# Kernel optimization log

Hardware: AMD Instinct MI355X
Metric: run time of the kernel (lower is better)

Reference implementation:

```python
import jax, jax.numpy as jnp
import numpy as np

ALPHA = 0.2  # LeakyReLU negative slope

def setup_inputs() -> dict:
    key = jax.random.key(0)
    k1, k2, k3 = jax.random.split(key, 3)
    B, N, D_in, D_out = 4, 512, 512, 256
    H = jax.random.normal(k1, (B, N, D_in), dtype=jnp.float32)
    # xavier-style scaled params
    W = jax.random.normal(k2, (D_out, D_in), dtype=jnp.float32) * (2.0 / (D_in + D_out)) ** 0.5
    a = jax.random.normal(k3, (D_out, 1), dtype=jnp.float32) * (2.0 / (D_out + 1)) ** 0.5
    return {"H": H, "W": W, "a": a}

def reference(H, W, a):
    # Wh: [B, N, D_out]
    Wh = jnp.einsum('bnd,od->bno', H, W)
    # additive pairwise scores: e[b,i,j] = leakyrelu(Wh[b,i]+Wh[b,j]) . a
    e = jnp.einsum('bijo,o->bij',
                   jax.nn.leaky_relu(Wh[:, :, None, :] + Wh[:, None, :, :], ALPHA),
                   a[:, 0])
    attention = jax.nn.softmax(e, axis=-1)          # [B, N, N]
    H_att = jnp.einsum('bij,bjo->bio', attention, Wh)  # [B, N, D_out]
    return H_att
```

## Files before the change

### kernel.cpp

```cpp
#include <hip/hip_runtime.h>

constexpr int Bq   = 4;
constexpr int Nq   = 512;
constexpr int DIN  = 512;
constexpr int DOUT = 256;

__device__ __forceinline__ void fma4(float4& acc, const float s, const float4 v) {
    acc.x = __builtin_fmaf(s, v.x, acc.x);
    acc.y = __builtin_fmaf(s, v.y, acc.y);
    acc.z = __builtin_fmaf(s, v.z, acc.z);
    acc.w = __builtin_fmaf(s, v.w, acc.w);
}

__global__ __launch_bounds__(256) void k0_wt(const float* __restrict__ W,
                                             float* __restrict__ WT) {
    __shared__ float tile[32][33];
    const int k0 = blockIdx.x * 32;
    const int o0 = blockIdx.y * 32;
    const int tx = threadIdx.x;
    const int ty = threadIdx.y;
#pragma unroll
    for (int j = 0; j < 4; ++j)
        tile[ty + 8 * j][tx] = W[(o0 + ty + 8 * j) * DIN + k0 + tx];
    __syncthreads();
#pragma unroll
    for (int j = 0; j < 4; ++j)
        WT[(k0 + ty + 8 * j) * DOUT + o0 + tx] = tile[tx][ty + 8 * j];
}

__global__ __launch_bounds__(512, 4) void k1_wh(const float* __restrict__ H,
                                                const float* __restrict__ WT,
                                                const float* __restrict__ a,
                                                float* __restrict__ Wh,
                                                float* __restrict__ WhT,
                                                float* __restrict__ r) {
    const int t   = threadIdx.x;
    const int blk = blockIdx.x;
    const int b   = blk & 3;
    const int n0  = (blk >> 2) << 2;
    const int p   = __builtin_amdgcn_readfirstlane(t >> 6);
    const int oq  = t & 63;

    __shared__ float  sH[4 * 512];
    __shared__ float4 sPart[8][4][64];

    {
        const float4* src = (const float4*)(H + ((size_t)(b * Nq) + n0) * DIN);
        ((float4*)sH)[t] = src[t];
    }
    __syncthreads();

    const float4* __restrict__ wt4 = (const float4*)WT + oq;

    float4 acc[4];
#pragma unroll
    for (int rr = 0; rr < 4; ++rr) acc[rr] = make_float4(0.f, 0.f, 0.f, 0.f);

    const int k0 = p * 64;
    float4 bufA[4], bufB[4];
#pragma unroll
    for (int s = 0; s < 4; ++s) bufA[s] = wt4[(k0 + s) * 64];

    for (int it = 0; it < 8; ++it) {
        const int kA = k0 + it * 8, kB = kA + 4;
#pragma unroll
        for (int s = 0; s < 4; ++s) bufB[s] = wt4[(kB + s) * 64];
#pragma unroll
        for (int rr = 0; rr < 4; ++rr) {
            const float4 h4 = *(const float4*)&sH[rr * 512 + kA];
            fma4(acc[rr], h4.x, bufA[0]); fma4(acc[rr], h4.y, bufA[1]);
            fma4(acc[rr], h4.z, bufA[2]); fma4(acc[rr], h4.w, bufA[3]);
        }
        if (it < 7) {
#pragma unroll
            for (int s = 0; s < 4; ++s) bufA[s] = wt4[(kA + 8 + s) * 64];
        }
#pragma unroll
        for (int rr = 0; rr < 4; ++rr) {
            const float4 h4 = *(const float4*)&sH[rr * 512 + kB];
            fma4(acc[rr], h4.x, bufB[0]); fma4(acc[rr], h4.y, bufB[1]);
            fma4(acc[rr], h4.z, bufB[2]); fma4(acc[rr], h4.w, bufB[3]);
        }
    }

#pragma unroll
    for (int rr = 0; rr < 4; ++rr) sPart[p][rr][oq] = acc[rr];
    __syncthreads();

    if (p < 4) {
        const int g = p;
        float4 fin = make_float4(0.f, 0.f, 0.f, 0.f);
#pragma unroll
        for (int pp = 0; pp < 8; ++pp) {
            const float4 v = sPart[pp][g][oq];
            fin.x += v.x; fin.y += v.y; fin.z += v.z; fin.w += v.w;
        }

        ((float4*)(Wh + ((size_t)(b * Nq) + n0 + g) * DOUT))[oq] = fin;

        float* wT = WhT + (size_t)b * DOUT * Nq;
        wT[(4 * oq + 0) * Nq + n0 + g] = fin.x;
        wT[(4 * oq + 1) * Nq + n0 + g] = fin.y;
        wT[(4 * oq + 2) * Nq + n0 + g] = fin.z;
        wT[(4 * oq + 3) * Nq + n0 + g] = fin.w;

        const float4 a4 = ((const float4*)a)[oq];
        float rp = a4.x * fin.x + a4.y * fin.y + a4.z * fin.z + a4.w * fin.w;
#pragma unroll
        for (int off = 32; off > 0; off >>= 1) rp += __shfl_xor(rp, off);
        if ((t & 63) == 0) r[(size_t)b * Nq + n0 + g] = rp;
    }
}

__global__ __launch_bounds__(1024, 4) void k2_attn(const float* __restrict__ Wh,
                                                   const float* __restrict__ WhT,
                                                   const float* __restrict__ a,
                                                   const float* __restrict__ r,
                                                   float* __restrict__ P) {
    const int t   = threadIdx.x;
    const int blk = blockIdx.x;
    const int b   = blk & 3;
    const int i0  = (blk >> 2) << 3;
    const int q   = __builtin_amdgcn_readfirstlane(t >> 8);
    const int jp  = t & 255;
    const int obase = q * 64;

    const float2* __restrict__ wj2 =
        (const float2*)(WhT + (size_t)b * DOUT * Nq + (size_t)obase * Nq) + jp;
    const float* __restrict__ gwi = Wh + ((size_t)b * Nq + i0) * DOUT;
    const float* __restrict__ gr  = r + (size_t)b * Nq;

    float ab0[8] = {0.f, 0.f, 0.f, 0.f, 0.f, 0.f, 0.f, 0.f};
    float ab1[8] = {0.f, 0.f, 0.f, 0.f, 0.f, 0.f, 0.f, 0.f};
    float2 bufA[8], bufB[8];

#pragma unroll
    for (int s = 0; s < 8; ++s) bufA[s] = wj2[s * 256];

    for (int cc = 0; cc < 4; ++cc) {
        const int oA = cc * 16, oB = oA + 8;
#pragma unroll
        for (int s = 0; s < 8; ++s) bufB[s] = wj2[(oB + s) * 256];
#pragma unroll
        for (int gg = 0; gg < 2; ++gg) {
            const int o4 = obase + oA + gg * 4;
            const float4 a4 = *(const float4*)(a + o4);
#pragma unroll
            for (int rr = 0; rr < 8; ++rr) {
                const float4 wi4 = *(const float4*)(gwi + rr * DOUT + o4);
#pragma unroll
                for (int s2 = 0; s2 < 4; ++s2) {
                    const float aq = ((const float*)&a4)[s2];
                    const float wi = ((const float*)&wi4)[s2];
                    const float2 wv = bufA[gg * 4 + s2];
                    ab0[rr] = __builtin_fmaf(aq, __builtin_fabsf(wi + wv.x), ab0[rr]);
                    ab1[rr] = __builtin_fmaf(aq, __builtin_fabsf(wi + wv.y), ab1[rr]);
                }
            }
        }
        if (cc < 3) {
#pragma unroll
            for (int s = 0; s < 8; ++s) bufA[s] = wj2[(oA + 16 + s) * 256];
        }
#pragma unroll
        for (int gg = 0; gg < 2; ++gg) {
            const int o4 = obase + oB + gg * 4;
            const float4 a4 = *(const float4*)(a + o4);
#pragma unroll
            for (int rr = 0; rr < 8; ++rr) {
                const float4 wi4 = *(const float4*)(gwi + rr * DOUT + o4);
#pragma unroll
                for (int s2 = 0; s2 < 4; ++s2) {
                    const float aq = ((const float*)&a4)[s2];
                    const float wi = ((const float*)&wi4)[s2];
                    const float2 wv = bufB[gg * 4 + s2];
                    ab0[rr] = __builtin_fmaf(aq, __builtin_fabsf(wi + wv.x), ab0[rr]);
                    ab1[rr] = __builtin_fmaf(aq, __builtin_fabsf(wi + wv.y), ab1[rr]);
                }
            }
        }
    }

    __shared__ float sAb[3][8][512];
    __shared__ float wred[2][8][4];
    if (q > 0) {
#pragma unroll
        for (int rr = 0; rr < 8; ++rr)
            ((float2*)&sAb[q - 1][rr][0])[jp] = make_float2(ab0[rr], ab1[rr]);
    }
    __syncthreads();

    float e0[8], e1[8];
    if (q == 0) {
        const float2 rj2 = ((const float2*)gr)[jp];
#pragma unroll
        for (int rr = 0; rr < 8; ++rr) {
            const float2 x0 = ((const float2*)&sAb[0][rr][0])[jp];
            const float2 x1 = ((const float2*)&sAb[1][rr][0])[jp];
            const float2 x2 = ((const float2*)&sAb[2][rr][0])[jp];
            const float A0 = ab0[rr] + x0.x + x1.x + x2.x;
            const float A1 = ab1[rr] + x0.y + x1.y + x2.y;
            const float ri = gr[i0 + rr];
            e0[rr] = 0.6f * (ri + rj2.x) + 0.4f * A0;
            e1[rr] = 0.6f * (ri + rj2.y) + 0.4f * A1;
        }
    }

    const int lane = t & 63;
    const int w    = (t >> 6) & 3;

#pragma unroll
    for (int rr = 0; rr < 8; ++rr) {
        float v = (q == 0) ? fmaxf(e0[rr], e1[rr]) : -3e38f;
#pragma unroll
        for (int off = 32; off > 0; off >>= 1) v = fmaxf(v, __shfl_xor(v, off));
        if (lane == 0 && q == 0) wred[0][rr][w] = v;
    }
    __syncthreads();

    float p0[8], p1[8];
    if (q == 0) {
#pragma unroll
        for (int rr = 0; rr < 8; ++rr) {
            const float4 qv = *(const float4*)&wred[0][rr][0];
            const float m = fmaxf(fmaxf(qv.x, qv.y), fmaxf(qv.z, qv.w));
            p0[rr] = __expf(e0[rr] - m);
            p1[rr] = __expf(e1[rr] - m);
        }
    }
#pragma unroll
    for (int rr = 0; rr < 8; ++rr) {
        float v = (q == 0) ? (p0[rr] + p1[rr]) : 0.f;
#pragma unroll
        for (int off = 32; off > 0; off >>= 1) v += __shfl_xor(v, off);
        if (lane == 0 && q == 0) wred[1][rr][w] = v;
    }
    __syncthreads();

    if (q == 0) {
        float2* prow = (float2*)(P + ((size_t)b * Nq + i0) * Nq) + jp;
#pragma unroll
        for (int rr = 0; rr < 8; ++rr) {
            const float4 qv = *(const float4*)&wred[1][rr][0];
            const float inv = 1.0f / (qv.x + qv.y + qv.z + qv.w);
            prow[rr * 256] = make_float2(p0[rr] * inv, p1[rr] * inv);
        }
    }
}

__global__ __launch_bounds__(512, 4) void k3_av(const float* __restrict__ Wh,
                                                const float* __restrict__ P,
                                                float* __restrict__ out) {
    const int t   = threadIdx.x;
    const int blk = blockIdx.x;
    const int b   = blk & 3;
    const int i0  = (blk >> 2) << 2;
    const int p   = __builtin_amdgcn_readfirstlane(t >> 6);
    const int oq  = t & 63;

    __shared__ float  sP[4 * 512];
    __shared__ float4 sPart[8][4][64];

    {
        const float4* src = (const float4*)(P + ((size_t)(b * Nq) + i0) * Nq);
        ((float4*)sP)[t] = src[t];
    }
    __syncthreads();

    const float4* __restrict__ wh4 = (const float4*)(Wh + (size_t)b * Nq * DOUT) + oq;

    float4 acc[4];
#pragma unroll
    for (int rr = 0; rr < 4; ++rr) acc[rr] = make_float4(0.f, 0.f, 0.f, 0.f);

    const int j0 = p * 64;
    float4 bufA[4], bufB[4];
#pragma unroll
    for (int s = 0; s < 4; ++s) bufA[s] = wh4[(j0 + s) * 64];

    for (int it = 0; it < 8; ++it) {
        const int jA = j0 + it * 8, jB = jA + 4;
#pragma unroll
        for (int s = 0; s < 4; ++s) bufB[s] = wh4[(jB + s) * 64];
#pragma unroll
        for (int rr = 0; rr < 4; ++rr) {
            const float4 p4 = *(const float4*)&sP[rr * 512 + jA];
            fma4(acc[rr], p4.x, bufA[0]); fma4(acc[rr], p4.y, bufA[1]);
            fma4(acc[rr], p4.z, bufA[2]); fma4(acc[rr], p4.w, bufA[3]);
        }
        if (it < 7) {
#pragma unroll
            for (int s = 0; s < 4; ++s) bufA[s] = wh4[(jA + 8 + s) * 64];
        }
#pragma unroll
        for (int rr = 0; rr < 4; ++rr) {
            const float4 p4 = *(const float4*)&sP[rr * 512 + jB];
            fma4(acc[rr], p4.x, bufB[0]); fma4(acc[rr], p4.y, bufB[1]);
            fma4(acc[rr], p4.z, bufB[2]); fma4(acc[rr], p4.w, bufB[3]);
        }
    }

#pragma unroll
    for (int rr = 0; rr < 4; ++rr) sPart[p][rr][oq] = acc[rr];
    __syncthreads();

    if (p < 4) {
        const int g = p;
        float4 fin = make_float4(0.f, 0.f, 0.f, 0.f);
#pragma unroll
        for (int pp = 0; pp < 8; ++pp) {
            const float4 v = sPart[pp][g][oq];
            fin.x += v.x; fin.y += v.y; fin.z += v.z; fin.w += v.w;
        }
        ((float4*)(out + ((size_t)(b * Nq) + i0 + g) * DOUT))[oq] = fin;
    }
}

extern "C" void kernel_launch(void* const* d_in, const int* in_sizes, int n_in,
                              void* d_out, int out_size, void* d_ws, size_t ws_size,
                              hipStream_t stream) {
    const float* H = (const float*)d_in[0];
    const float* W = (const float*)d_in[1];
    const float* a = (const float*)d_in[2];
    float* out = (float*)d_out;

    float* Wh  = (float*)d_ws;
    float* WhT = Wh  + Bq * Nq * DOUT;
    float* P   = WhT + Bq * Nq * DOUT;
    float* WT  = P;
    float* r   = out;

    hipLaunchKernelGGL(k0_wt,   dim3(16, 8), dim3(32, 8), 0, stream, W, WT);
    hipLaunchKernelGGL(k1_wh,   dim3(512),   dim3(512),   0, stream, H, WT, a, Wh, WhT, r);
    hipLaunchKernelGGL(k2_attn, dim3(256),   dim3(1024),  0, stream, Wh, WhT, a, r, P);
    hipLaunchKernelGGL(k3_av,   dim3(512),   dim3(512),   0, stream, Wh, P, out);
}
```

Measured before the change: 121.9 us.

## Fuse attention scores, softmax and attention-value product into one kernel

```diff
diff --git a/kernel.cpp b/kernel.cpp
--- a/kernel.cpp
+++ b/kernel.cpp
@@ -5,11 +5,12 @@
 constexpr int DIN  = 512;
 constexpr int DOUT = 256;
 
-__device__ __forceinline__ void fma4(float4& acc, const float s, const float4 v) {
-    acc.x = __builtin_fmaf(s, v.x, acc.x);
-    acc.y = __builtin_fmaf(s, v.y, acc.y);
-    acc.z = __builtin_fmaf(s, v.z, acc.z);
-    acc.w = __builtin_fmaf(s, v.w, acc.w);
+typedef float v2f __attribute__((ext_vector_type(2)));
+typedef float v4f __attribute__((ext_vector_type(4)));
+
+__device__ __forceinline__ v4f fma4v(const float s, const v4f v, const v4f acc) {
+    v4f sv = s;
+    return __builtin_elementwise_fma(sv, v, acc);
 }
 
 __global__ __launch_bounds__(256) void k0_wt(const float* __restrict__ W,
@@ -41,23 +42,23 @@
     const int p   = __builtin_amdgcn_readfirstlane(t >> 6);
     const int oq  = t & 63;
 
-    __shared__ float  sH[4 * 512];
-    __shared__ float4 sPart[8][4][64];
+    __shared__ float sH[4 * 512];
+    __shared__ v4f   sPart[8][4][64];
 
     {
-        const float4* src = (const float4*)(H + ((size_t)(b * Nq) + n0) * DIN);
-        ((float4*)sH)[t] = src[t];
+        const v4f* src = (const v4f*)(H + ((size_t)(b * Nq) + n0) * DIN);
+        ((v4f*)sH)[t] = src[t];
     }
     __syncthreads();
 
-    const float4* __restrict__ wt4 = (const float4*)WT + oq;
-
-    float4 acc[4];
-#pragma unroll
-    for (int rr = 0; rr < 4; ++rr) acc[rr] = make_float4(0.f, 0.f, 0.f, 0.f);
+    const v4f* __restrict__ wt4 = (const v4f*)WT + oq;
+
+    v4f acc[4];
+#pragma unroll
+    for (int rr = 0; rr < 4; ++rr) acc[rr] = (v4f)0.f;
 
     const int k0 = p * 64;
-    float4 bufA[4], bufB[4];
+    v4f bufA[4], bufB[4];
 #pragma unroll
     for (int s = 0; s < 4; ++s) bufA[s] = wt4[(k0 + s) * 64];
 
@@ -67,9 +68,11 @@
         for (int s = 0; s < 4; ++s) bufB[s] = wt4[(kB + s) * 64];
 #pragma unroll
         for (int rr = 0; rr < 4; ++rr) {
-            const float4 h4 = *(const float4*)&sH[rr * 512 + kA];
-            fma4(acc[rr], h4.x, bufA[0]); fma4(acc[rr], h4.y, bufA[1]);
-            fma4(acc[rr], h4.z, bufA[2]); fma4(acc[rr], h4.w, bufA[3]);
+            const v4f h4 = *(const v4f*)&sH[rr * 512 + kA];
+            acc[rr] = fma4v(h4.x, bufA[0], acc[rr]);
+            acc[rr] = fma4v(h4.y, bufA[1], acc[rr]);
+            acc[rr] = fma4v(h4.z, bufA[2], acc[rr]);
+            acc[rr] = fma4v(h4.w, bufA[3], acc[rr]);
         }
         if (it < 7) {
 #pragma unroll
@@ -77,9 +80,11 @@
         }
 #pragma unroll
         for (int rr = 0; rr < 4; ++rr) {
-            const float4 h4 = *(const float4*)&sH[rr * 512 + kB];
-            fma4(acc[rr], h4.x, bufB[0]); fma4(acc[rr], h4.y, bufB[1]);
-            fma4(acc[rr], h4.z, bufB[2]); fma4(acc[rr], h4.w, bufB[3]);
+            const v4f h4 = *(const v4f*)&sH[rr * 512 + kB];
+            acc[rr] = fma4v(h4.x, bufB[0], acc[rr]);
+            acc[rr] = fma4v(h4.y, bufB[1], acc[rr]);
+            acc[rr] = fma4v(h4.z, bufB[2], acc[rr]);
+            acc[rr] = fma4v(h4.w, bufB[3], acc[rr]);
         }
     }
 
@@ -89,14 +94,11 @@
 
     if (p < 4) {
         const int g = p;
-        float4 fin = make_float4(0.f, 0.f, 0.f, 0.f);
-#pragma unroll
-        for (int pp = 0; pp < 8; ++pp) {
-            const float4 v = sPart[pp][g][oq];
-            fin.x += v.x; fin.y += v.y; fin.z += v.z; fin.w += v.w;
-        }
-
-        ((float4*)(Wh + ((size_t)(b * Nq) + n0 + g) * DOUT))[oq] = fin;
+        v4f fin = (v4f)0.f;
+#pragma unroll
+        for (int pp = 0; pp < 8; ++pp) fin += sPart[pp][g][oq];
+
+        ((v4f*)(Wh + ((size_t)(b * Nq) + n0 + g) * DOUT))[oq] = fin;
 
         float* wT = WhT + (size_t)b * DOUT * Nq;
         wT[(4 * oq + 0) * Nq + n0 + g] = fin.x;
@@ -104,7 +106,7 @@
         wT[(4 * oq + 2) * Nq + n0 + g] = fin.z;
         wT[(4 * oq + 3) * Nq + n0 + g] = fin.w;
 
-        const float4 a4 = ((const float4*)a)[oq];
+        const v4f a4 = ((const v4f*)a)[oq];
         float rp = a4.x * fin.x + a4.y * fin.y + a4.z * fin.z + a4.w * fin.w;
 #pragma unroll
         for (int off = 32; off > 0; off >>= 1) rp += __shfl_xor(rp, off);
@@ -112,207 +114,220 @@
     }
 }
 
-__global__ __launch_bounds__(1024, 4) void k2_attn(const float* __restrict__ Wh,
-                                                   const float* __restrict__ WhT,
-                                                   const float* __restrict__ a,
-                                                   const float* __restrict__ r,
-                                                   float* __restrict__ P) {
+__global__ __launch_bounds__(1024, 4) void k23(const float* __restrict__ Wh,
+                                               const float* __restrict__ WhT,
+                                               const float* __restrict__ a,
+                                               const float* __restrict__ r,
+                                               float* __restrict__ out) {
     const int t   = threadIdx.x;
     const int blk = blockIdx.x;
     const int b   = blk & 3;
     const int i0  = (blk >> 2) << 3;
-    const int q   = __builtin_amdgcn_readfirstlane(t >> 8);
-    const int jp  = t & 255;
-    const int obase = q * 64;
-
-    const float2* __restrict__ wj2 =
-        (const float2*)(WhT + (size_t)b * DOUT * Nq + (size_t)obase * Nq) + jp;
-    const float* __restrict__ gwi = Wh + ((size_t)b * Nq + i0) * DOUT;
-    const float* __restrict__ gr  = r + (size_t)b * Nq;
-
-    float ab0[8] = {0.f, 0.f, 0.f, 0.f, 0.f, 0.f, 0.f, 0.f};
-    float ab1[8] = {0.f, 0.f, 0.f, 0.f, 0.f, 0.f, 0.f, 0.f};
-    float2 bufA[8], bufB[8];
-
-#pragma unroll
-    for (int s = 0; s < 8; ++s) bufA[s] = wj2[s * 256];
-
-    for (int cc = 0; cc < 4; ++cc) {
-        const int oA = cc * 16, oB = oA + 8;
-#pragma unroll
-        for (int s = 0; s < 8; ++s) bufB[s] = wj2[(oB + s) * 256];
-#pragma unroll
-        for (int gg = 0; gg < 2; ++gg) {
-            const int o4 = obase + oA + gg * 4;
-            const float4 a4 = *(const float4*)(a + o4);
+
+    __shared__ float smem[8192];
+    __shared__ float sP[8 * 512];
+    __shared__ float wred[2][8][4];
+
+    {
+        const int q  = __builtin_amdgcn_readfirstlane(t >> 8);
+        const int jp = t & 255;
+        const int obase = q * 64;
+
+        const v2f* __restrict__ wj2 =
+            (const v2f*)(WhT + (size_t)b * DOUT * Nq + (size_t)obase * Nq) + jp;
+        const float* __restrict__ gwi = Wh + ((size_t)b * Nq + i0) * DOUT;
+        const float* __restrict__ gr  = r + (size_t)b * Nq;
+
+        v2f ab[8];
+#pragma unroll
+        for (int rr = 0; rr < 8; ++rr) ab[rr] = (v2f)0.f;
+        v2f bufA[8], bufB[8];
+
+#pragma unroll
+        for (int s = 0; s < 8; ++s) bufA[s] = wj2[s * 256];
+
+        for (int cc = 0; cc < 4; ++cc) {
+            const int oA = cc * 16, oB = oA + 8;
+#pragma unroll
+            for (int s = 0; s < 8; ++s) bufB[s] = wj2[(oB + s) * 256];
+#pragma unroll
+            for (int gg = 0; gg < 2; ++gg) {
+                const int o4 = obase + oA + gg * 4;
+                const float4 a4 = *(const float4*)(a + o4);
+#pragma unroll
+                for (int rr = 0; rr < 8; ++rr) {
+                    const float4 wi4 = *(const float4*)(gwi + rr * DOUT + o4);
+#pragma unroll
+                    for (int s2 = 0; s2 < 4; ++s2) {
+                        const float aq = ((const float*)&a4)[s2];
+                        const float wi = ((const float*)&wi4)[s2];
+                        v2f w  = bufA[gg * 4 + s2] + wi;
+                        v2f aw = __builtin_elementwise_max(w, -w);
+                        v2f av = aq;
+                        ab[rr] = __builtin_elementwise_fma(av, aw, ab[rr]);
+                    }
+                }
+            }
+            if (cc < 3) {
+#pragma unroll
+                for (int s = 0; s < 8; ++s) bufA[s] = wj2[(oA + 16 + s) * 256];
+            }
+#pragma unroll
+            for (int gg = 0; gg < 2; ++gg) {
+                const int o4 = obase + oB + gg * 4;
+                const float4 a4 = *(const float4*)(a + o4);
+#pragma unroll
+                for (int rr = 0; rr < 8; ++rr) {
+                    const float4 wi4 = *(const float4*)(gwi + rr * DOUT + o4);
+#pragma unroll
+                    for (int s2 = 0; s2 < 4; ++s2) {
+                        const float aq = ((const float*)&a4)[s2];
+                        const float wi = ((const float*)&wi4)[s2];
+                        v2f w  = bufB[gg * 4 + s2] + wi;
+                        v2f aw = __builtin_elementwise_max(w, -w);
+                        v2f av = aq;
+                        ab[rr] = __builtin_elementwise_fma(av, aw, ab[rr]);
+                    }
+                }
+            }
+        }
+
+        v2f* sAb = (v2f*)smem;
+        if (q >= 2) {
+#pragma unroll
+            for (int rr = 0; rr < 8; ++rr) sAb[((q - 2) * 8 + rr) * 256 + jp] = ab[rr];
+        }
+        __syncthreads();
+        if (q < 2) {
+#pragma unroll
+            for (int rr = 0; rr < 8; ++rr) ab[rr] += sAb[(q * 8 + rr) * 256 + jp];
+        }
+        __syncthreads();
+        if (q == 1) {
+#pragma unroll
+            for (int rr = 0; rr < 8; ++rr) sAb[(0 * 8 + rr) * 256 + jp] = ab[rr];
+        }
+        __syncthreads();
+
+        float e0[8], e1[8];
+        if (q == 0) {
+            const v2f rj2 = ((const v2f*)gr)[jp];
 #pragma unroll
             for (int rr = 0; rr < 8; ++rr) {
-                const float4 wi4 = *(const float4*)(gwi + rr * DOUT + o4);
-#pragma unroll
-                for (int s2 = 0; s2 < 4; ++s2) {
-                    const float aq = ((const float*)&a4)[s2];
-                    const float wi = ((const float*)&wi4)[s2];
-                    const float2 wv = bufA[gg * 4 + s2];
-                    ab0[rr] = __builtin_fmaf(aq, __builtin_fabsf(wi + wv.x), ab0[rr]);
-                    ab1[rr] = __builtin_fmaf(aq, __builtin_fabsf(wi + wv.y), ab1[rr]);
-                }
-            }
-        }
-        if (cc < 3) {
-#pragma unroll
-            for (int s = 0; s < 8; ++s) bufA[s] = wj2[(oA + 16 + s) * 256];
-        }
-#pragma unroll
-        for (int gg = 0; gg < 2; ++gg) {
-            const int o4 = obase + oB + gg * 4;
-            const float4 a4 = *(const float4*)(a + o4);
+                const v2f x = sAb[(0 * 8 + rr) * 256 + jp];
+                const float A0 = ab[rr].x + x.x;
+                const float A1 = ab[rr].y + x.y;
+                const float ri = gr[i0 + rr];
+                e0[rr] = 0.6f * (ri + rj2.x) + 0.4f * A0;
+                e1[rr] = 0.6f * (ri + rj2.y) + 0.4f * A1;
+            }
+        }
+
+        const int lane = t & 63;
+        const int w    = (t >> 6) & 3;
+
+#pragma unroll
+        for (int rr = 0; rr < 8; ++rr) {
+            float v = (q == 0) ? fmaxf(e0[rr], e1[rr]) : -3e38f;
+#pragma unroll
+            for (int off = 32; off > 0; off >>= 1) v = fmaxf(v, __shfl_xor(v, off));
+            if (lane == 0 && q == 0) wred[0][rr][w] = v;
+        }
+        __syncthreads();
+
+        float p0[8], p1[8];
+        if (q == 0) {
 #pragma unroll
             for (int rr = 0; rr < 8; ++rr) {
-                const float4 wi4 = *(const float4*)(gwi + rr * DOUT + o4);
-#pragma unroll
-                for (int s2 = 0; s2 < 4; ++s2) {
-                    const float aq = ((const float*)&a4)[s2];
-                    const float wi = ((const float*)&wi4)[s2];
-                    const float2 wv = bufB[gg * 4 + s2];
-                    ab0[rr] = __builtin_fmaf(aq, __builtin_fabsf(wi + wv.x), ab0[rr]);
-                    ab1[rr] = __builtin_fmaf(aq, __builtin_fabsf(wi + wv.y), ab1[rr]);
-                }
-            }
-        }
-    }
-
-    __shared__ float sAb[3][8][512];
-    __shared__ float wred[2][8][4];
-    if (q > 0) {
-#pragma unroll
-        for (int rr = 0; rr < 8; ++rr)
-            ((float2*)&sAb[q - 1][rr][0])[jp] = make_float2(ab0[rr], ab1[rr]);
-    }
-    __syncthreads();
-
-    float e0[8], e1[8];
-    if (q == 0) {
-        const float2 rj2 = ((const float2*)gr)[jp];
+                const float4 qv = *(const float4*)&wred[0][rr][0];
+                const float m = fmaxf(fmaxf(qv.x, qv.y), fmaxf(qv.z, qv.w));
+                p0[rr] = __expf(e0[rr] - m);
+                p1[rr] = __expf(e1[rr] - m);
+            }
+        }
 #pragma unroll
         for (int rr = 0; rr < 8; ++rr) {
-            const float2 x0 = ((const float2*)&sAb[0][rr][0])[jp];
-            const float2 x1 = ((const float2*)&sAb[1][rr][0])[jp];
-            const float2 x2 = ((const float2*)&sAb[2][rr][0])[jp];
-            const float A0 = ab0[rr] + x0.x + x1.x + x2.x;
-            const float A1 = ab1[rr] + x0.y + x1.y + x2.y;
-            const float ri = gr[i0 + rr];
-            e0[rr] = 0.6f * (ri + rj2.x) + 0.4f * A0;
-            e1[rr] = 0.6f * (ri + rj2.y) + 0.4f * A1;
-        }
-    }
-
-    const int lane = t & 63;
-    const int w    = (t >> 6) & 3;
-
-#pragma unroll
-    for (int rr = 0; rr < 8; ++rr) {
-        float v = (q == 0) ? fmaxf(e0[rr], e1[rr]) : -3e38f;
-#pragma unroll
-        for (int off = 32; off > 0; off >>= 1) v = fmaxf(v, __shfl_xor(v, off));
-        if (lane == 0 && q == 0) wred[0][rr][w] = v;
-    }
-    __syncthreads();
-
-    float p0[8], p1[8];
-    if (q == 0) {
-#pragma unroll
-        for (int rr = 0; rr < 8; ++rr) {
-            const float4 qv = *(const float4*)&wred[0][rr][0];
-            const float m = fmaxf(fmaxf(qv.x, qv.y), fmaxf(qv.z, qv.w));
-            p0[rr] = __expf(e0[rr] - m);
-            p1[rr] = __expf(e1[rr] - m);
-        }
-    }
-#pragma unroll
-    for (int rr = 0; rr < 8; ++rr) {
-        float v = (q == 0) ? (p0[rr] + p1[rr]) : 0.f;
-#pragma unroll
-        for (int off = 32; off > 0; off >>= 1) v += __shfl_xor(v, off);
-        if (lane == 0 && q == 0) wred[1][rr][w] = v;
-    }
-    __syncthreads();
-
-    if (q == 0) {
-        float2* prow = (float2*)(P + ((size_t)b * Nq + i0) * Nq) + jp;
-#pragma unroll
-        for (int rr = 0; rr < 8; ++rr) {
-            const float4 qv = *(const float4*)&wred[1][rr][0];
-            const float inv = 1.0f / (qv.x + qv.y + qv.z + qv.w);
-            prow[rr * 256] = make_float2(p0[rr] * inv, p1[rr] * inv);
-        }
-    }
-}
-
-__global__ __launch_bounds__(512, 4) void k3_av(const float* __restrict__ Wh,
-                                                const float* __restrict__ P,
-                                                float* __restrict__ out) {
-    const int t   = threadIdx.x;
-    const int blk = blockIdx.x;
-    const int b   = blk & 3;
-    const int i0  = (blk >> 2) << 2;
-    const int p   = __builtin_amdgcn_readfirstlane(t >> 6);
-    const int oq  = t & 63;
-
-    __shared__ float  sP[4 * 512];
-    __shared__ float4 sPart[8][4][64];
+            float v = (q == 0) ? (p0[rr] + p1[rr]) : 0.f;
+#pragma unroll
+            for (int off = 32; off > 0; off >>= 1) v += __shfl_xor(v, off);
+            if (lane == 0 && q == 0) wred[1][rr][w] = v;
+        }
+        __syncthreads();
+
+        if (q == 0) {
+#pragma unroll
+            for (int rr = 0; rr < 8; ++rr) {
+                const float4 qv = *(const float4*)&wred[1][rr][0];
+                const float inv = 1.0f / (qv.x + qv.y + qv.z + qv.w);
+                ((v2f*)sP)[rr * 256 + jp] = (v2f){p0[rr] * inv, p1[rr] * inv};
+            }
+        }
+        __syncthreads();
+    }
 
     {
-        const float4* src = (const float4*)(P + ((size_t)(b * Nq) + i0) * Nq);
-        ((float4*)sP)[t] = src[t];
-    }
-    __syncthreads();
-
-    const float4* __restrict__ wh4 = (const float4*)(Wh + (size_t)b * Nq * DOUT) + oq;
-
-    float4 acc[4];
-#pragma unroll
-    for (int rr = 0; rr < 4; ++rr) acc[rr] = make_float4(0.f, 0.f, 0.f, 0.f);
-
-    const int j0 = p * 64;
-    float4 bufA[4], bufB[4];
-#pragma unroll
-    for (int s = 0; s < 4; ++s) bufA[s] = wh4[(j0 + s) * 64];
-
-    for (int it = 0; it < 8; ++it) {
-        const int jA = j0 + it * 8, jB = jA + 4;
-#pragma unroll
-        for (int s = 0; s < 4; ++s) bufB[s] = wh4[(jB + s) * 64];
-#pragma unroll
-        for (int rr = 0; rr < 4; ++rr) {
-            const float4 p4 = *(const float4*)&sP[rr * 512 + jA];
-            fma4(acc[rr], p4.x, bufA[0]); fma4(acc[rr], p4.y, bufA[1]);
-            fma4(acc[rr], p4.z, bufA[2]); fma4(acc[rr], p4.w, bufA[3]);
-        }
-        if (it < 7) {
-#pragma unroll
-            for (int s = 0; s < 4; ++s) bufA[s] = wh4[(jA + 8 + s) * 64];
-        }
-#pragma unroll
-        for (int rr = 0; rr < 4; ++rr) {
-            const float4 p4 = *(const float4*)&sP[rr * 512 + jB];
-            fma4(acc[rr], p4.x, bufB[0]); fma4(acc[rr], p4.y, bufB[1]);
-            fma4(acc[rr], p4.z, bufB[2]); fma4(acc[rr], p4.w, bufB[3]);
-        }
-    }
-
-#pragma unroll
-    for (int rr = 0; rr < 4; ++rr) sPart[p][rr][oq] = acc[rr];
-    __syncthreads();
-
-    if (p < 4) {
-        const int g = p;
-        float4 fin = make_float4(0.f, 0.f, 0.f, 0.f);
-#pragma unroll
-        for (int pp = 0; pp < 8; ++pp) {
-            const float4 v = sPart[pp][g][oq];
-            fin.x += v.x; fin.y += v.y; fin.z += v.z; fin.w += v.w;
-        }
-        ((float4*)(out + ((size_t)(b * Nq) + i0 + g) * DOUT))[oq] = fin;
+        const int p2 = __builtin_amdgcn_readfirstlane(t >> 6);
+        const int jh = p2 & 7;
+        const int rh = p2 >> 3;
+        const int oq = t & 63;
+
+        const v4f* __restrict__ wh4 = (const v4f*)(Wh + (size_t)b * Nq * DOUT) + oq;
+
+        v4f acc[4];
+#pragma unroll
+        for (int rr = 0; rr < 4; ++rr) acc[rr] = (v4f)0.f;
+
+        const int j0 = jh * 64;
+        v4f bufA[4], bufB[4];
+#pragma unroll
+        for (int s = 0; s < 4; ++s) bufA[s] = wh4[(j0 + s) * 64];
+
+        for (int it = 0; it < 8; ++it) {
+            const int jA = j0 + it * 8, jB = jA + 4;
+#pragma unroll
+            for (int s = 0; s < 4; ++s) bufB[s] = wh4[(jB + s) * 64];
+#pragma unroll
+            for (int rr = 0; rr < 4; ++rr) {
+                const v4f p4 = *(const v4f*)&sP[(rh * 4 + rr) * 512 + jA];
+                acc[rr] = fma4v(p4.x, bufA[0], acc[rr]);
+                acc[rr] = fma4v(p4.y, bufA[1], acc[rr]);
+                acc[rr] = fma4v(p4.z, bufA[2], acc[rr]);
+                acc[rr] = fma4v(p4.w, bufA[3], acc[rr]);
+            }
+            if (it < 7) {
+#pragma unroll
+                for (int s = 0; s < 4; ++s) bufA[s] = wh4[(jA + 8 + s) * 64];
+            }
+#pragma unroll
+            for (int rr = 0; rr < 4; ++rr) {
+                const v4f p4 = *(const v4f*)&sP[(rh * 4 + rr) * 512 + jB];
+                acc[rr] = fma4v(p4.x, bufB[0], acc[rr]);
+                acc[rr] = fma4v(p4.y, bufB[1], acc[rr]);
+                acc[rr] = fma4v(p4.z, bufB[2], acc[rr]);
+                acc[rr] = fma4v(p4.w, bufB[3], acc[rr]);
+            }
+        }
+
+        v4f* sPart = (v4f*)smem;
+        if (jh < 4) {
+#pragma unroll
+            for (int rr = 0; rr < 4; ++rr)
+                sPart[(jh * 8 + rh * 4 + rr) * 64 + oq] = acc[rr];
+        }
+        __syncthreads();
+        if (jh >= 4) {
+#pragma unroll
+            for (int rr = 0; rr < 4; ++rr)
+                sPart[((jh - 4) * 8 + rh * 4 + rr) * 64 + oq] += acc[rr];
+        }
+        __syncthreads();
+
+        if (p2 < 8) {
+            const int row = p2;
+            v4f fin = sPart[(0 * 8 + row) * 64 + oq] + sPart[(1 * 8 + row) * 64 + oq]
+                    + sPart[(2 * 8 + row) * 64 + oq] + sPart[(3 * 8 + row) * 64 + oq];
+            ((v4f*)(out + ((size_t)(b * Nq) + i0 + row) * DOUT))[oq] = fin;
+        }
     }
 }
 
@@ -326,12 +341,10 @@
 
     float* Wh  = (float*)d_ws;
     float* WhT = Wh  + Bq * Nq * DOUT;
-    float* P   = WhT + Bq * Nq * DOUT;
-    float* WT  = P;
-    float* r   = out;
-
-    hipLaunchKernelGGL(k0_wt,   dim3(16, 8), dim3(32, 8), 0, stream, W, WT);
-    hipLaunchKernelGGL(k1_wh,   dim3(512),   dim3(512),   0, stream, H, WT, a, Wh, WhT, r);
-    hipLaunchKernelGGL(k2_attn, dim3(256),   dim3(1024),  0, stream, Wh, WhT, a, r, P);
-    hipLaunchKernelGGL(k3_av,   dim3(512),   dim3(512),   0, stream, Wh, P, out);
-}
+    float* r   = WhT + Bq * Nq * DOUT;
+    float* WT  = r   + Bq * Nq;
+
+    hipLaunchKernelGGL(k0_wt, dim3(16, 8), dim3(32, 8), 0, stream, W, WT);
+    hipLaunchKernelGGL(k1_wh, dim3(512),   dim3(512),   0, stream, H, WT, a, Wh, WhT, r);
+    hipLaunchKernelGGL(k23,   dim3(256),   dim3(1024),  0, stream, Wh, WhT, a, r, out);
+}
```

Measured after the change: 115.5 us. 5.3% less time.
